# Performance work log

Hardware: AMD Instinct MI355X
Metric: run time of the kernel (lower is better)

The kernel has to match this reference:

```python
import jax, jax.numpy as jnp
import numpy as np

N_FULL = 50000
N_POOL = 12500
E_FULL = 600000
E_POOL = 150000
D = 128


def gcn_conv(x, W, b, edge_index, n):
    """GCNConv with self-loops and symmetric normalization.
    x: [n, d_in], W: [d_in, d_out], edge_index: [2, E] (src -> dst)."""
    xw = x @ W  # [n, d_out]
    loops = jnp.arange(n, dtype=edge_index.dtype)
    src = jnp.concatenate([edge_index[0], loops])
    dst = jnp.concatenate([edge_index[1], loops])
    deg = jnp.zeros((n,), dtype=xw.dtype).at[dst].add(1.0)  # >= 1 (self loops)
    dinv = jax.lax.rsqrt(deg)
    norm = (dinv[src] * dinv[dst])[:, None]  # [E+n, 1]
    out = jax.ops.segment_sum(xw[src] * norm, dst, num_segments=n)
    return out + b


def setup_inputs() -> dict:
    key = jax.random.key(0)
    ks = jax.random.split(key, 8)
    s = 1.0 / np.sqrt(D)
    return {
        "x": jnp.zeros((N_FULL, D), jnp.float32),
        "edge_index": jax.random.randint(ks[0], (2, E_FULL), 0, N_FULL, dtype=jnp.int64)
            if jax.config.jax_enable_x64 else jax.random.randint(ks[0], (2, E_FULL), 0, N_FULL).astype(jnp.int32),
        "pooled_x": jax.random.normal(ks[1], (N_POOL, D), jnp.float32),
        "pooled_edge_index": jax.random.randint(ks[2], (2, E_POOL), 0, N_POOL).astype(jnp.int32),
        "unpool_info": jnp.arange(N_POOL, dtype=jnp.int32),  # unique TopK-kept indices
        "W0": jax.random.normal(ks[3], (D, D), jnp.float32) * s,
        "b0": jnp.zeros((D,), jnp.float32),
        "W1": jax.random.normal(ks[4], (D, D), jnp.float32) * s,
        "b1": jnp.zeros((D,), jnp.float32),
        "W2": jax.random.normal(ks[5], (D, D), jnp.float32) * s,
        "b2": jnp.zeros((D,), jnp.float32),
    }


def reference(x, edge_index, pooled_x, pooled_edge_index, unpool_info,
              W0, b0, W1, b1, W2, b2):
    n = x.shape[0]
    # conv0 on the pooled graph + activation (ELU)
    h = jax.nn.elu(gcn_conv(pooled_x, W0, b0, pooled_edge_index, pooled_x.shape[0]))
    # TopKPool unpool: zero full graph, scatter pooled features to kept indices
    xf = jnp.zeros_like(x).at[unpool_info].set(h)
    # remaining convs on the full graph (dropout=0 / eval mode -> identity)
    xf = jax.nn.elu(gcn_conv(xf, W1, b1, edge_index, n))
    xf = jax.nn.elu(gcn_conv(xf, W2, b2, edge_index, n))
    return xf
```

## Files before the change

### kernel.cpp

```cpp
#include <hip/hip_runtime.h>
#include <math.h>

#define DD 128
#define CF 48
#define CP 48
#define OVF_CAP 4096

static inline int cdiv(long a, long b){ return (int)((a + b - 1) / b); }

typedef __attribute__((ext_vector_type(4))) float f32x4;
typedef __attribute__((ext_vector_type(8))) short bf16x8;
typedef __attribute__((ext_vector_type(4))) short sh4;

__device__ __forceinline__ unsigned short bf16_rn(float f){
  unsigned u = __float_as_uint(f);
  u += 0x7fffu + ((u >> 16) & 1u);
  return (unsigned short)(u >> 16);
}

__global__ void k_scatter(const int* __restrict__ src_f, const int* __restrict__ dst_f, int Ef,
                          int* __restrict__ cnt_f, int* __restrict__ ewk_f,
                          int2* __restrict__ ovf_f, int* __restrict__ novf_f,
                          const int* __restrict__ src_p, const int* __restrict__ dst_p, int Ep,
                          int* __restrict__ cnt_p, int* __restrict__ ewk_p,
                          int2* __restrict__ ovf_p, int* __restrict__ novf_p,
                          const int* __restrict__ unpool, int* __restrict__ inv, int npool){
  int e = blockIdx.x * blockDim.x + threadIdx.x;
  if (e < Ef){
    int s = src_f[e], d = dst_f[e];
    int r = atomicAdd(&cnt_f[d], 1);
    if (r < CF) ewk_f[(long)d * CF + r] = s;
    else { int o = atomicAdd(novf_f, 1); if (o < OVF_CAP) ovf_f[o] = make_int2(s, d); }
    return;
  }
  e -= Ef;
  if (e < Ep){
    int s = src_p[e], d = dst_p[e];
    int r = atomicAdd(&cnt_p[d], 1);
    if (r < CP) ewk_p[(long)d * CP + r] = s;
    else { int o = atomicAdd(novf_p, 1); if (o < OVF_CAP) ovf_p[o] = make_int2(s, d); }
    return;
  }
  e -= Ep;
  if (e < npool) inv[unpool[e]] = e;
}

template <int AMODE, bool BF16OUT>
__global__ __launch_bounds__(256, 2) void k_gemm_mfma(const void* __restrict__ Ap,
                                                      const float* __restrict__ W,
                                                      void* __restrict__ Cout, int n){
  __shared__ unsigned short Wl[2][16384];
  const int t    = threadIdx.x;
  const int lane = t & 63;
  const int wv   = t >> 6;
  const int g    = lane >> 4;
  const int r    = lane & 15;

  #pragma unroll
  for (int i = 0; i < 4; i++){
    int item = t + i * 256;
    int kq = item >> 5;
    int c4 = item & 31;
    const float* Wp = W + (long)kq * 512 + c4 * 4;
    float4 ww[4];
    #pragma unroll
    for (int kk = 0; kk < 4; kk++) ww[kk] = *(const float4*)(Wp + kk * 128);
    #pragma unroll
    for (int m = 0; m < 4; m++){
      int c = c4 * 4 + m;
      int boff = c * 256 + (((kq >> 1) ^ (c & 15)) * 16) + (kq & 1) * 8;
      sh4 hq, lq;
      #pragma unroll
      for (int kk = 0; kk < 4; kk++){
        float f = ((const float*)&ww[kk])[m];
        unsigned short hh = bf16_rn(f);
        float hf = __uint_as_float((unsigned)hh << 16);
        hq[kk] = (short)hh;
        lq[kk] = (short)bf16_rn(f - hf);
      }
      *(sh4*)((char*)(&Wl[0][0]) + boff) = hq;
      *(sh4*)((char*)(&Wl[1][0]) + boff) = lq;
    }
  }
  __syncthreads();

  const int rb = blockIdx.x * 128 + wv * 32;
  const int r0 = rb + r, r1 = rb + 16 + r;
  const bool v0 = r0 < n, v1 = r1 < n;

  f32x4 acc[2][8];
  #pragma unroll
  for (int i = 0; i < 2; i++)
    #pragma unroll
    for (int j = 0; j < 8; j++){ f32x4 z = {0.f,0.f,0.f,0.f}; acc[i][j] = z; }

  #pragma unroll
  for (int ks = 0; ks < 4; ks++){
    bf16x8 ah0, al0, ah1, al1;
    if (AMODE == 0){
      const float* pa0 = (const float*)Ap + (long)r0 * DD + g * 8;
      const float* pa1 = (const float*)Ap + (long)r1 * DD + g * 8;
      const float4 z4 = make_float4(0.f,0.f,0.f,0.f);
      float4 a00 = v0 ? *(const float4*)(pa0 + ks * 32)     : z4;
      float4 a01 = v0 ? *(const float4*)(pa0 + ks * 32 + 4) : z4;
      float4 a10 = v1 ? *(const float4*)(pa1 + ks * 32)     : z4;
      float4 a11 = v1 ? *(const float4*)(pa1 + ks * 32 + 4) : z4;
      float f0[8] = {a00.x,a00.y,a00.z,a00.w,a01.x,a01.y,a01.z,a01.w};
      float f1[8] = {a10.x,a10.y,a10.z,a10.w,a11.x,a11.y,a11.z,a11.w};
      #pragma unroll
      for (int i = 0; i < 8; i++){
        unsigned short hh = bf16_rn(f0[i]);
        ah0[i] = (short)hh;
        al0[i] = (short)bf16_rn(f0[i] - __uint_as_float((unsigned)hh << 16));
        unsigned short h1 = bf16_rn(f1[i]);
        ah1[i] = (short)h1;
        al1[i] = (short)bf16_rn(f1[i] - __uint_as_float((unsigned)h1 << 16));
      }
    } else {
      const unsigned* qa0 = (const unsigned*)Ap + (long)r0 * DD + g * 8;
      const unsigned* qa1 = (const unsigned*)Ap + (long)r1 * DD + g * 8;
      const uint4 z4 = make_uint4(0,0,0,0);
      uint4 u00 = v0 ? *(const uint4*)(qa0 + ks * 32)     : z4;
      uint4 u01 = v0 ? *(const uint4*)(qa0 + ks * 32 + 4) : z4;
      uint4 u10 = v1 ? *(const uint4*)(qa1 + ks * 32)     : z4;
      uint4 u11 = v1 ? *(const uint4*)(qa1 + ks * 32 + 4) : z4;
      unsigned uu0[8] = {u00.x,u00.y,u00.z,u00.w,u01.x,u01.y,u01.z,u01.w};
      unsigned uu1[8] = {u10.x,u10.y,u10.z,u10.w,u11.x,u11.y,u11.z,u11.w};
      #pragma unroll
      for (int i = 0; i < 8; i++){
        ah0[i] = (short)(uu0[i] & 0xffffu); al0[i] = (short)(uu0[i] >> 16);
        ah1[i] = (short)(uu1[i] & 0xffffu); al1[i] = (short)(uu1[i] >> 16);
      }
    }
    const int sb = ks * 4 + g;
    #pragma unroll
    for (int cf = 0; cf < 8; cf++){
      const int boff = (cf * 16 + r) * 256 + ((sb ^ r) * 16);
      bf16x8 wh = *(const bf16x8*)((const char*)(&Wl[0][0]) + boff);
      bf16x8 wl = *(const bf16x8*)((const char*)(&Wl[1][0]) + boff);
      acc[0][cf] = __builtin_amdgcn_mfma_f32_16x16x32_bf16(ah0, wh, acc[0][cf], 0, 0, 0);
      acc[1][cf] = __builtin_amdgcn_mfma_f32_16x16x32_bf16(ah1, wh, acc[1][cf], 0, 0, 0);
      acc[0][cf] = __builtin_amdgcn_mfma_f32_16x16x32_bf16(al0, wh, acc[0][cf], 0, 0, 0);
      acc[1][cf] = __builtin_amdgcn_mfma_f32_16x16x32_bf16(al1, wh, acc[1][cf], 0, 0, 0);
      acc[0][cf] = __builtin_amdgcn_mfma_f32_16x16x32_bf16(ah0, wl, acc[0][cf], 0, 0, 0);
      acc[1][cf] = __builtin_amdgcn_mfma_f32_16x16x32_bf16(ah1, wl, acc[1][cf], 0, 0, 0);
    }
  }

  #pragma unroll
  for (int rf = 0; rf < 2; rf++){
    #pragma unroll
    for (int cf = 0; cf < 8; cf++){
      #pragma unroll
      for (int e = 0; e < 4; e++){
        int row = rb + rf * 16 + g * 4 + e;
        if (row < n){
          float v = acc[rf][cf][e];
          if (BF16OUT)
            ((unsigned short*)Cout)[(long)row * DD + cf * 16 + r] = bf16_rn(v);
          else
            ((float*)Cout)[(long)row * DD + cf * 16 + r] = v;
        }
      }
    }
  }
}

__global__ __launch_bounds__(256) void k_agg0(const float* __restrict__ xw,
    const int* __restrict__ cnt, const int* __restrict__ ewk,
    const int2* __restrict__ ovf, const int* __restrict__ novf,
    const float* __restrict__ b, unsigned* __restrict__ outp, int n){
  int row = blockIdx.x * 4 + (threadIdx.x >> 6);
  if (row >= n) return;
  int c = (threadIdx.x & 63) * 2;
  int deg = __builtin_amdgcn_readfirstlane(cnt[row]);
  int m = deg < CP ? deg : CP;
  long base = (long)row * CP;
  float ax[4], ay[4];
  #pragma unroll
  for (int i = 0; i < 4; i++){ ax[i] = 0.f; ay[i] = 0.f; }
  int j = 0;
  for (; j + 3 < m; j += 4){
    int4 ss = *(const int4*)(ewk + base + j);
    int sa[4] = {ss.x, ss.y, ss.z, ss.w};
    #pragma unroll
    for (int i = 0; i < 4; i++){
      int s = sa[i];
      float w = rsqrtf((float)cnt[s] + 1.f);
      float2 v = *(const float2*)(xw + (long)s * DD + c);
      ax[i] += v.x * w; ay[i] += v.y * w;
    }
  }
  for (; j < m; j++){
    int s = ewk[base + j];
    float w = rsqrtf((float)cnt[s] + 1.f);
    float2 v = *(const float2*)(xw + (long)s * DD + c);
    ax[0] += v.x * w; ay[0] += v.y * w;
  }
  int no = __builtin_amdgcn_readfirstlane(novf[0]);
  if (no > 0){
    no = no < OVF_CAP ? no : OVF_CAP;
    for (int k = 0; k < no; k++){
      int2 od = ovf[k];
      if (od.y == row){
        float w = rsqrtf((float)cnt[od.x] + 1.f);
        float2 v = *(const float2*)(xw + (long)od.x * DD + c);
        ax[0] += v.x * w; ay[0] += v.y * w;
      }
    }
  }
  float sax = (ax[0]+ax[1]) + (ax[2]+ax[3]);
  float say = (ay[0]+ay[1]) + (ay[2]+ay[3]);
  float dd = rsqrtf((float)deg + 1.f);
  float2 sv = *(const float2*)(xw + (long)row * DD + c);
  float2 bb = *(const float2*)(b + c);
  float vx = sax * dd + sv.x * dd * dd + bb.x;
  float vy = say * dd + sv.y * dd * dd + bb.y;
  vx = vx > 0.f ? vx : expm1f(vx);
  vy = vy > 0.f ? vy : expm1f(vy);
  unsigned short hx = bf16_rn(vx);
  unsigned short lx = bf16_rn(vx - __uint_as_float((unsigned)hx << 16));
  unsigned short hy = bf16_rn(vy);
  unsigned short ly = bf16_rn(vy - __uint_as_float((unsigned)hy << 16));
  *(uint2*)(outp + (long)row * DD + c) =
      make_uint2((unsigned)hx | ((unsigned)lx << 16), (unsigned)hy | ((unsigned)ly << 16));
}

__global__ __launch_bounds__(256) void k_agg1(const unsigned short* __restrict__ hwb,
    const int* __restrict__ inv, const int* __restrict__ cnt,
    const int* __restrict__ ewk, const int2* __restrict__ ovf, const int* __restrict__ novf,
    const float* __restrict__ b, unsigned* __restrict__ outp, int n){
  int row = blockIdx.x * 4 + (threadIdx.x >> 6);
  if (row >= n) return;
  int c = (threadIdx.x & 63) * 2;
  int deg = __builtin_amdgcn_readfirstlane(cnt[row]);
  int m = deg < CF ? deg : CF;
  long base = (long)row * CF;
  float ax[8], ay[8];
  #pragma unroll
  for (int i = 0; i < 8; i++){ ax[i] = 0.f; ay[i] = 0.f; }
  int j = 0;
  for (; j + 7 < m; j += 8){
    int4 s0 = *(const int4*)(ewk + base + j);
    int4 s1 = *(const int4*)(ewk + base + j + 4);
    int sa[8] = {s0.x, s0.y, s0.z, s0.w, s1.x, s1.y, s1.z, s1.w};
    #pragma unroll
    for (int i = 0; i < 8; i++){
      int s = sa[i];
      int pr = inv[s];
      if (pr >= 0){
        float w = rsqrtf((float)cnt[s] + 1.f);
        unsigned v = *(const unsigned*)(hwb + (long)pr * DD + c);
        ax[i] += __uint_as_float(v << 16) * w;
        ay[i] += __uint_as_float(v & 0xffff0000u) * w;
      }
    }
  }
  for (; j < m; j++){
    int s = ewk[base + j];
    int pr = inv[s];
    if (pr >= 0){
      float w = rsqrtf((float)cnt[s] + 1.f);
      unsigned v = *(const unsigned*)(hwb + (long)pr * DD + c);
      ax[0] += __uint_as_float(v << 16) * w;
      ay[0] += __uint_as_float(v & 0xffff0000u) * w;
    }
  }
  int no = __builtin_amdgcn_readfirstlane(novf[0]);
  if (no > 0){
    no = no < OVF_CAP ? no : OVF_CAP;
    for (int k = 0; k < no; k++){
      int2 od = ovf[k];
      if (od.y == row){
        int pr = inv[od.x];
        if (pr >= 0){
          float w = rsqrtf((float)cnt[od.x] + 1.f);
          unsigned v = *(const unsigned*)(hwb + (long)pr * DD + c);
          ax[0] += __uint_as_float(v << 16) * w;
          ay[0] += __uint_as_float(v & 0xffff0000u) * w;
        }
      }
    }
  }
  float sax = ((ax[0]+ax[1])+(ax[2]+ax[3])) + ((ax[4]+ax[5])+(ax[6]+ax[7]));
  float say = ((ay[0]+ay[1])+(ay[2]+ay[3])) + ((ay[4]+ay[5])+(ay[6]+ay[7]));
  float dd = rsqrtf((float)deg + 1.f);
  int pr = inv[row];
  float sx = 0.f, sy = 0.f;
  if (pr >= 0){
    unsigned sv = *(const unsigned*)(hwb + (long)pr * DD + c);
    sx = __uint_as_float(sv << 16); sy = __uint_as_float(sv & 0xffff0000u);
  }
  float2 bb = *(const float2*)(b + c);
  float vx = sax * dd + sx * dd * dd + bb.x;
  float vy = say * dd + sy * dd * dd + bb.y;
  vx = vx > 0.f ? vx : expm1f(vx);
  vy = vy > 0.f ? vy : expm1f(vy);
  unsigned short hx = bf16_rn(vx);
  unsigned short lx = bf16_rn(vx - __uint_as_float((unsigned)hx << 16));
  unsigned short hy = bf16_rn(vy);
  unsigned short ly = bf16_rn(vy - __uint_as_float((unsigned)hy << 16));
  *(uint2*)(outp + (long)row * DD + c) =
      make_uint2((unsigned)hx | ((unsigned)lx << 16), (unsigned)hy | ((unsigned)ly << 16));
}

__global__ __launch_bounds__(256) void k_agg2(const unsigned short* __restrict__ xwb,
    const int* __restrict__ cnt, const int* __restrict__ ewk,
    const int2* __restrict__ ovf, const int* __restrict__ novf,
    const float* __restrict__ b, float* __restrict__ out, int n){
  int row = blockIdx.x * 4 + (threadIdx.x >> 6);
  if (row >= n) return;
  int c = (threadIdx.x & 63) * 2;
  int deg = __builtin_amdgcn_readfirstlane(cnt[row]);
  int m = deg < CF ? deg : CF;
  long base = (long)row * CF;
  float ax[8], ay[8];
  #pragma unroll
  for (int i = 0; i < 8; i++){ ax[i] = 0.f; ay[i] = 0.f; }
  int j = 0;
  for (; j + 7 < m; j += 8){
    int4 s0 = *(const int4*)(ewk + base + j);
    int4 s1 = *(const int4*)(ewk + base + j + 4);
    int sa[8] = {s0.x, s0.y, s0.z, s0.w, s1.x, s1.y, s1.z, s1.w};
    #pragma unroll
    for (int i = 0; i < 8; i++){
      int s = sa[i];
      float w = rsqrtf((float)cnt[s] + 1.f);
      unsigned v = *(const unsigned*)(xwb + (long)s * DD + c);
      ax[i] += __uint_as_float(v << 16) * w;
      ay[i] += __uint_as_float(v & 0xffff0000u) * w;
    }
  }
  for (; j < m; j++){
    int s = ewk[base + j];
    float w = rsqrtf((float)cnt[s] + 1.f);
    unsigned v = *(const unsigned*)(xwb + (long)s * DD + c);
    ax[0] += __uint_as_float(v << 16) * w;
    ay[0] += __uint_as_float(v & 0xffff0000u) * w;
  }
  int no = __builtin_amdgcn_readfirstlane(novf[0]);
  if (no > 0){
    no = no < OVF_CAP ? no : OVF_CAP;
    for (int k = 0; k < no; k++){
      int2 od = ovf[k];
      if (od.y == row){
        float w = rsqrtf((float)cnt[od.x] + 1.f);
        unsigned v = *(const unsigned*)(xwb + (long)od.x * DD + c);
        ax[0] += __uint_as_float(v << 16) * w;
        ay[0] += __uint_as_float(v & 0xffff0000u) * w;
      }
    }
  }
  float sax = ((ax[0]+ax[1])+(ax[2]+ax[3])) + ((ax[4]+ax[5])+(ax[6]+ax[7]));
  float say = ((ay[0]+ay[1])+(ay[2]+ay[3])) + ((ay[4]+ay[5])+(ay[6]+ay[7]));
  float dd = rsqrtf((float)deg + 1.f);
  unsigned sv = *(const unsigned*)(xwb + (long)row * DD + c);
  float sx = __uint_as_float(sv << 16), sy = __uint_as_float(sv & 0xffff0000u);
  float2 bb = *(const float2*)(b + c);
  float vx = sax * dd + sx * dd * dd + bb.x;
  float vy = say * dd + sy * dd * dd + bb.y;
  vx = vx > 0.f ? vx : expm1f(vx);
  vy = vy > 0.f ? vy : expm1f(vy);
  *(float2*)(out + (long)row * DD + c) = make_float2(vx, vy);
}

extern "C" void kernel_launch(void* const* d_in, const int* in_sizes, int n_in,
                              void* d_out, int out_size, void* d_ws, size_t ws_size,
                              hipStream_t stream) {
  const int*   edge   = (const int*)d_in[1];
  const float* px     = (const float*)d_in[2];
  const int*   pedge  = (const int*)d_in[3];
  const int*   unpool = (const int*)d_in[4];
  const float* W0 = (const float*)d_in[5]; const float* b0 = (const float*)d_in[6];
  const float* W1 = (const float*)d_in[7]; const float* b1 = (const float*)d_in[8];
  const float* W2 = (const float*)d_in[9]; const float* b2 = (const float*)d_in[10];
  const int n_full = in_sizes[0] / DD;
  const int E_full = in_sizes[1] / 2;
  const int n_pool = in_sizes[2] / DD;
  const int E_pool = in_sizes[3] / 2;
  float* out = (float*)d_out;

  char* w = (char*)d_ws;
  size_t off = 0;
  auto alloc = [&](size_t bytes) -> void* {
    void* p = (void*)(w + off);
    off += (bytes + 255) / 256 * 256;
    return p;
  };
  int* cnt_p  = (int*)alloc((size_t)n_pool * 4);
  int* cnt_f  = (int*)alloc((size_t)n_full * 4);
  int* novf2  = (int*)alloc(8);
  size_t zspan = (size_t)((char*)(novf2 + 2) - (char*)cnt_p);
  int* invm   = (int*)alloc((size_t)n_full * 4);
  int* ewk_p  = (int*)alloc((size_t)n_pool * CP * 4);
  int* ewk_f  = (int*)alloc((size_t)n_full * CF * 4);
  int2* ovf_p = (int2*)alloc((size_t)OVF_CAP * 8);
  int2* ovf_f = (int2*)alloc((size_t)OVF_CAP * 8);
  const size_t big = (size_t)n_full * DD * 4;
  float* bufA = (float*)alloc(big);
  float* bufB = (float*)alloc(big);

  const int* src_f = edge;          const int* dst_f = edge + E_full;
  const int* src_p = pedge;         const int* dst_p = pedge + E_pool;

  (void)hipMemsetAsync(cnt_p, 0, zspan, stream);
  (void)hipMemsetAsync(invm, 0xFF, (size_t)n_full * 4, stream);
  k_scatter<<<cdiv((long)E_full + E_pool + n_pool, 256), 256, 0, stream>>>(
      src_f, dst_f, E_full, cnt_f, ewk_f, ovf_f, novf2 + 1,
      src_p, dst_p, E_pool, cnt_p, ewk_p, ovf_p, novf2 + 0,
      unpool, invm, n_pool);

  float* xw0            = bufA;
  unsigned* h0p         = (unsigned*)bufB;
  unsigned short* hw1b  = (unsigned short*)bufA;
  unsigned* y1p         = (unsigned*)bufB;
  unsigned short* xw2b  = (unsigned short*)bufA;

  k_gemm_mfma<0,false><<<cdiv(n_pool,128),256,0,stream>>>(px, W0, xw0, n_pool);
  k_agg0<<<cdiv(n_pool,4),256,0,stream>>>(xw0, cnt_p, ewk_p, ovf_p, novf2 + 0, b0, h0p, n_pool);

  k_gemm_mfma<1,true><<<cdiv(n_pool,128),256,0,stream>>>(h0p, W1, hw1b, n_pool);
  k_agg1<<<cdiv(n_full,4),256,0,stream>>>(hw1b, invm, cnt_f, ewk_f, ovf_f, novf2 + 1, b1, y1p, n_full);

  k_gemm_mfma<1,true><<<cdiv(n_full,128),256,0,stream>>>(y1p, W2, xw2b, n_full);
  k_agg2<<<cdiv(n_full,4),256,0,stream>>>(xw2b, cnt_f, ewk_f, ovf_f, novf2 + 1, b2, out, n_full);
}
```

Measured before the change: 297.4 us.

## Precompute edge weights and filtered pooled-source adjacency in a two-pass build

Splits the adjacency build into a degree-count pass and a fill pass. The fill pass stores (src, rsqrt(deg+1)) pairs so the aggregation kernels no longer do a dependent cnt[] lookup and rsqrt per edge. It also builds a separate compact list for the conv1 aggregation that holds only edges whose source is a kept pooled node, already remapped to its pooled row, which removes the inv[] indirection and the wasted iterations over dropped sources. The cost is an extra kernel launch, a second pass over the edge list with more atomics, and adjacency entries twice as wide.

```diff
diff --git a/kernel.cpp b/kernel.cpp
--- a/kernel.cpp
+++ b/kernel.cpp
@@ -3,7 +3,7 @@
 
 #define DD 128
 #define CF 48
-#define CP 48
+#define C1 16
 #define OVF_CAP 4096
 
 static inline int cdiv(long a, long b){ return (int)((a + b - 1) / b); }
@@ -18,31 +18,50 @@
   return (unsigned short)(u >> 16);
 }
 
-__global__ void k_scatter(const int* __restrict__ src_f, const int* __restrict__ dst_f, int Ef,
-                          int* __restrict__ cnt_f, int* __restrict__ ewk_f,
-                          int2* __restrict__ ovf_f, int* __restrict__ novf_f,
-                          const int* __restrict__ src_p, const int* __restrict__ dst_p, int Ep,
-                          int* __restrict__ cnt_p, int* __restrict__ ewk_p,
-                          int2* __restrict__ ovf_p, int* __restrict__ novf_p,
-                          const int* __restrict__ unpool, int* __restrict__ inv, int npool){
+__global__ void k_count(const int* __restrict__ dst_f, int Ef, int* __restrict__ cnt_f,
+                        const int* __restrict__ dst_p, int Ep, int* __restrict__ cnt_p,
+                        const int* __restrict__ unpool, int* __restrict__ inv, int npool){
+  int e = blockIdx.x * blockDim.x + threadIdx.x;
+  if (e < Ef){ atomicAdd(&cnt_f[dst_f[e]], 1); return; }
+  e -= Ef;
+  if (e < Ep){ atomicAdd(&cnt_p[dst_p[e]], 1); return; }
+  e -= Ep;
+  if (e < npool) inv[unpool[e]] = e;
+}
+
+__global__ void k_fill(const int* __restrict__ src_f, const int* __restrict__ dst_f, int Ef,
+                       const int* __restrict__ cnt_f, const int* __restrict__ invm,
+                       int* __restrict__ rk2, int2* __restrict__ ew2,
+                       int4* __restrict__ ovf2, int* __restrict__ novf2,
+                       int* __restrict__ rk1, int2* __restrict__ ew1,
+                       int4* __restrict__ ovf1, int* __restrict__ novf1,
+                       const int* __restrict__ src_p, const int* __restrict__ dst_p, int Ep,
+                       const int* __restrict__ cnt_p,
+                       int* __restrict__ rk0, int2* __restrict__ ew0,
+                       int4* __restrict__ ovf0, int* __restrict__ novf0){
   int e = blockIdx.x * blockDim.x + threadIdx.x;
   if (e < Ef){
     int s = src_f[e], d = dst_f[e];
-    int r = atomicAdd(&cnt_f[d], 1);
-    if (r < CF) ewk_f[(long)d * CF + r] = s;
-    else { int o = atomicAdd(novf_f, 1); if (o < OVF_CAP) ovf_f[o] = make_int2(s, d); }
+    int w = __float_as_int(rsqrtf((float)cnt_f[s] + 1.f));
+    int r = atomicAdd(&rk2[d], 1);
+    if (r < CF) ew2[(long)d * CF + r] = make_int2(s, w);
+    else { int o = atomicAdd(novf2, 1); if (o < OVF_CAP) ovf2[o] = make_int4(s, w, d, 0); }
+    int pr = invm[s];
+    if (pr >= 0){
+      int r1 = atomicAdd(&rk1[d], 1);
+      if (r1 < C1) ew1[(long)d * C1 + r1] = make_int2(pr, w);
+      else { int o = atomicAdd(novf1, 1); if (o < OVF_CAP) ovf1[o] = make_int4(pr, w, d, 0); }
+    }
     return;
   }
   e -= Ef;
   if (e < Ep){
     int s = src_p[e], d = dst_p[e];
-    int r = atomicAdd(&cnt_p[d], 1);
-    if (r < CP) ewk_p[(long)d * CP + r] = s;
-    else { int o = atomicAdd(novf_p, 1); if (o < OVF_CAP) ovf_p[o] = make_int2(s, d); }
-    return;
-  }
-  e -= Ep;
-  if (e < npool) inv[unpool[e]] = e;
+    int w = __float_as_int(rsqrtf((float)cnt_p[s] + 1.f));
+    int r = atomicAdd(&rk0[d], 1);
+    if (r < CF) ew0[(long)d * CF + r] = make_int2(s, w);
+    else { int o = atomicAdd(novf0, 1); if (o < OVF_CAP) ovf0[o] = make_int4(s, w, d, 0); }
+  }
 }
 
 template <int AMODE, bool BF16OUT>
@@ -167,43 +186,44 @@
 }
 
 __global__ __launch_bounds__(256) void k_agg0(const float* __restrict__ xw,
-    const int* __restrict__ cnt, const int* __restrict__ ewk,
-    const int2* __restrict__ ovf, const int* __restrict__ novf,
+    const int* __restrict__ cnt, const int2* __restrict__ ew,
+    const int4* __restrict__ ovf, const int* __restrict__ novf,
     const float* __restrict__ b, unsigned* __restrict__ outp, int n){
   int row = blockIdx.x * 4 + (threadIdx.x >> 6);
   if (row >= n) return;
   int c = (threadIdx.x & 63) * 2;
   int deg = __builtin_amdgcn_readfirstlane(cnt[row]);
-  int m = deg < CP ? deg : CP;
-  long base = (long)row * CP;
+  int m = deg < CF ? deg : CF;
+  long base = (long)row * CF;
   float ax[4], ay[4];
   #pragma unroll
   for (int i = 0; i < 4; i++){ ax[i] = 0.f; ay[i] = 0.f; }
   int j = 0;
   for (; j + 3 < m; j += 4){
-    int4 ss = *(const int4*)(ewk + base + j);
-    int sa[4] = {ss.x, ss.y, ss.z, ss.w};
+    const int4* qp = (const int4*)(ew + base + j);
+    int4 q0 = qp[0], q1 = qp[1];
+    int sa[4] = {q0.x, q0.z, q1.x, q1.z};
+    int wa[4] = {q0.y, q0.w, q1.y, q1.w};
     #pragma unroll
     for (int i = 0; i < 4; i++){
-      int s = sa[i];
-      float w = rsqrtf((float)cnt[s] + 1.f);
-      float2 v = *(const float2*)(xw + (long)s * DD + c);
+      float w = __int_as_float(wa[i]);
+      float2 v = *(const float2*)(xw + (long)sa[i] * DD + c);
       ax[i] += v.x * w; ay[i] += v.y * w;
     }
   }
   for (; j < m; j++){
-    int s = ewk[base + j];
-    float w = rsqrtf((float)cnt[s] + 1.f);
-    float2 v = *(const float2*)(xw + (long)s * DD + c);
+    int2 q = ew[base + j];
+    float w = __int_as_float(q.y);
+    float2 v = *(const float2*)(xw + (long)q.x * DD + c);
     ax[0] += v.x * w; ay[0] += v.y * w;
   }
   int no = __builtin_amdgcn_readfirstlane(novf[0]);
   if (no > 0){
     no = no < OVF_CAP ? no : OVF_CAP;
     for (int k = 0; k < no; k++){
-      int2 od = ovf[k];
-      if (od.y == row){
-        float w = rsqrtf((float)cnt[od.x] + 1.f);
+      int4 od = ovf[k];
+      if (od.z == row){
+        float w = __int_as_float(od.y);
         float2 v = *(const float2*)(xw + (long)od.x * DD + c);
         ax[0] += v.x * w; ay[0] += v.y * w;
       }
@@ -227,65 +247,58 @@
 }
 
 __global__ __launch_bounds__(256) void k_agg1(const unsigned short* __restrict__ hwb,
-    const int* __restrict__ inv, const int* __restrict__ cnt,
-    const int* __restrict__ ewk, const int2* __restrict__ ovf, const int* __restrict__ novf,
+    const int* __restrict__ invm, const int* __restrict__ cnt_f,
+    const int* __restrict__ rk1, const int2* __restrict__ ew,
+    const int4* __restrict__ ovf, const int* __restrict__ novf,
     const float* __restrict__ b, unsigned* __restrict__ outp, int n){
   int row = blockIdx.x * 4 + (threadIdx.x >> 6);
   if (row >= n) return;
   int c = (threadIdx.x & 63) * 2;
-  int deg = __builtin_amdgcn_readfirstlane(cnt[row]);
-  int m = deg < CF ? deg : CF;
-  long base = (long)row * CF;
-  float ax[8], ay[8];
-  #pragma unroll
-  for (int i = 0; i < 8; i++){ ax[i] = 0.f; ay[i] = 0.f; }
+  int m1 = __builtin_amdgcn_readfirstlane(rk1[row]);
+  if (m1 > C1) m1 = C1;
+  int deg = __builtin_amdgcn_readfirstlane(cnt_f[row]);
+  long base = (long)row * C1;
+  float ax[4], ay[4];
+  #pragma unroll
+  for (int i = 0; i < 4; i++){ ax[i] = 0.f; ay[i] = 0.f; }
   int j = 0;
-  for (; j + 7 < m; j += 8){
-    int4 s0 = *(const int4*)(ewk + base + j);
-    int4 s1 = *(const int4*)(ewk + base + j + 4);
-    int sa[8] = {s0.x, s0.y, s0.z, s0.w, s1.x, s1.y, s1.z, s1.w};
-    #pragma unroll
-    for (int i = 0; i < 8; i++){
-      int s = sa[i];
-      int pr = inv[s];
-      if (pr >= 0){
-        float w = rsqrtf((float)cnt[s] + 1.f);
-        unsigned v = *(const unsigned*)(hwb + (long)pr * DD + c);
-        ax[i] += __uint_as_float(v << 16) * w;
-        ay[i] += __uint_as_float(v & 0xffff0000u) * w;
-      }
-    }
-  }
-  for (; j < m; j++){
-    int s = ewk[base + j];
-    int pr = inv[s];
-    if (pr >= 0){
-      float w = rsqrtf((float)cnt[s] + 1.f);
-      unsigned v = *(const unsigned*)(hwb + (long)pr * DD + c);
-      ax[0] += __uint_as_float(v << 16) * w;
-      ay[0] += __uint_as_float(v & 0xffff0000u) * w;
-    }
+  for (; j + 3 < m1; j += 4){
+    const int4* qp = (const int4*)(ew + base + j);
+    int4 q0 = qp[0], q1 = qp[1];
+    int sa[4] = {q0.x, q0.z, q1.x, q1.z};
+    int wa[4] = {q0.y, q0.w, q1.y, q1.w};
+    #pragma unroll
+    for (int i = 0; i < 4; i++){
+      float w = __int_as_float(wa[i]);
+      unsigned v = *(const unsigned*)(hwb + (long)sa[i] * DD + c);
+      ax[i] += __uint_as_float(v << 16) * w;
+      ay[i] += __uint_as_float(v & 0xffff0000u) * w;
+    }
+  }
+  for (; j < m1; j++){
+    int2 q = ew[base + j];
+    float w = __int_as_float(q.y);
+    unsigned v = *(const unsigned*)(hwb + (long)q.x * DD + c);
+    ax[0] += __uint_as_float(v << 16) * w;
+    ay[0] += __uint_as_float(v & 0xffff0000u) * w;
   }
   int no = __builtin_amdgcn_readfirstlane(novf[0]);
   if (no > 0){
     no = no < OVF_CAP ? no : OVF_CAP;
     for (int k = 0; k < no; k++){
-      int2 od = ovf[k];
-      if (od.y == row){
-        int pr = inv[od.x];
-        if (pr >= 0){
-          float w = rsqrtf((float)cnt[od.x] + 1.f);
-          unsigned v = *(const unsigned*)(hwb + (long)pr * DD + c);
-          ax[0] += __uint_as_float(v << 16) * w;
-          ay[0] += __uint_as_float(v & 0xffff0000u) * w;
-        }
-      }
-    }
-  }
-  float sax = ((ax[0]+ax[1])+(ax[2]+ax[3])) + ((ax[4]+ax[5])+(ax[6]+ax[7]));
-  float say = ((ay[0]+ay[1])+(ay[2]+ay[3])) + ((ay[4]+ay[5])+(ay[6]+ay[7]));
+      int4 od = ovf[k];
+      if (od.z == row){
+        float w = __int_as_float(od.y);
+        unsigned v = *(const unsigned*)(hwb + (long)od.x * DD + c);
+        ax[0] += __uint_as_float(v << 16) * w;
+        ay[0] += __uint_as_float(v & 0xffff0000u) * w;
+      }
+    }
+  }
+  float sax = (ax[0]+ax[1]) + (ax[2]+ax[3]);
+  float say = (ay[0]+ay[1]) + (ay[2]+ay[3]);
   float dd = rsqrtf((float)deg + 1.f);
-  int pr = inv[row];
+  int pr = invm[row];
   float sx = 0.f, sy = 0.f;
   if (pr >= 0){
     unsigned sv = *(const unsigned*)(hwb + (long)pr * DD + c);
@@ -305,8 +318,8 @@
 }
 
 __global__ __launch_bounds__(256) void k_agg2(const unsigned short* __restrict__ xwb,
-    const int* __restrict__ cnt, const int* __restrict__ ewk,
-    const int2* __restrict__ ovf, const int* __restrict__ novf,
+    const int* __restrict__ cnt, const int2* __restrict__ ew,
+    const int4* __restrict__ ovf, const int* __restrict__ novf,
     const float* __restrict__ b, float* __restrict__ out, int n){
   int row = blockIdx.x * 4 + (threadIdx.x >> 6);
   if (row >= n) return;
@@ -319,22 +332,22 @@
   for (int i = 0; i < 8; i++){ ax[i] = 0.f; ay[i] = 0.f; }
   int j = 0;
   for (; j + 7 < m; j += 8){
-    int4 s0 = *(const int4*)(ewk + base + j);
-    int4 s1 = *(const int4*)(ewk + base + j + 4);
-    int sa[8] = {s0.x, s0.y, s0.z, s0.w, s1.x, s1.y, s1.z, s1.w};
+    const int4* qp = (const int4*)(ew + base + j);
+    int4 q0 = qp[0], q1 = qp[1], q2 = qp[2], q3 = qp[3];
+    int sa[8] = {q0.x, q0.z, q1.x, q1.z, q2.x, q2.z, q3.x, q3.z};
+    int wa[8] = {q0.y, q0.w, q1.y, q1.w, q2.y, q2.w, q3.y, q3.w};
     #pragma unroll
     for (int i = 0; i < 8; i++){
-      int s = sa[i];
-      float w = rsqrtf((float)cnt[s] + 1.f);
-      unsigned v = *(const unsigned*)(xwb + (long)s * DD + c);
+      float w = __int_as_float(wa[i]);
+      unsigned v = *(const unsigned*)(xwb + (long)sa[i] * DD + c);
       ax[i] += __uint_as_float(v << 16) * w;
       ay[i] += __uint_as_float(v & 0xffff0000u) * w;
     }
   }
   for (; j < m; j++){
-    int s = ewk[base + j];
-    float w = rsqrtf((float)cnt[s] + 1.f);
-    unsigned v = *(const unsigned*)(xwb + (long)s * DD + c);
+    int2 q = ew[base + j];
+    float w = __int_as_float(q.y);
+    unsigned v = *(const unsigned*)(xwb + (long)q.x * DD + c);
     ax[0] += __uint_as_float(v << 16) * w;
     ay[0] += __uint_as_float(v & 0xffff0000u) * w;
   }
@@ -342,9 +355,9 @@
   if (no > 0){
     no = no < OVF_CAP ? no : OVF_CAP;
     for (int k = 0; k < no; k++){
-      int2 od = ovf[k];
-      if (od.y == row){
-        float w = rsqrtf((float)cnt[od.x] + 1.f);
+      int4 od = ovf[k];
+      if (od.z == row){
+        float w = __int_as_float(od.y);
         unsigned v = *(const unsigned*)(xwb + (long)od.x * DD + c);
         ax[0] += __uint_as_float(v << 16) * w;
         ay[0] += __uint_as_float(v & 0xffff0000u) * w;
@@ -387,15 +400,20 @@
     off += (bytes + 255) / 256 * 256;
     return p;
   };
-  int* cnt_p  = (int*)alloc((size_t)n_pool * 4);
-  int* cnt_f  = (int*)alloc((size_t)n_full * 4);
-  int* novf2  = (int*)alloc(8);
-  size_t zspan = (size_t)((char*)(novf2 + 2) - (char*)cnt_p);
-  int* invm   = (int*)alloc((size_t)n_full * 4);
-  int* ewk_p  = (int*)alloc((size_t)n_pool * CP * 4);
-  int* ewk_f  = (int*)alloc((size_t)n_full * CF * 4);
-  int2* ovf_p = (int2*)alloc((size_t)OVF_CAP * 8);
-  int2* ovf_f = (int2*)alloc((size_t)OVF_CAP * 8);
+  int* cnt_f = (int*)alloc((size_t)n_full * 4);
+  int* cnt_p = (int*)alloc((size_t)n_pool * 4);
+  int* rk2   = (int*)alloc((size_t)n_full * 4);
+  int* rk1   = (int*)alloc((size_t)n_full * 4);
+  int* rk0   = (int*)alloc((size_t)n_pool * 4);
+  int* novf3 = (int*)alloc(12);
+  size_t zspan = (size_t)((char*)(novf3 + 3) - (char*)cnt_f);
+  int* invm  = (int*)alloc((size_t)n_full * 4);
+  int2* ew2  = (int2*)alloc((size_t)n_full * CF * 8);
+  int2* ew1  = (int2*)alloc((size_t)n_full * C1 * 8);
+  int2* ew0  = (int2*)alloc((size_t)n_pool * CF * 8);
+  int4* ovf2 = (int4*)alloc((size_t)OVF_CAP * 16);
+  int4* ovf1 = (int4*)alloc((size_t)OVF_CAP * 16);
+  int4* ovf0 = (int4*)alloc((size_t)OVF_CAP * 16);
   const size_t big = (size_t)n_full * DD * 4;
   float* bufA = (float*)alloc(big);
   float* bufB = (float*)alloc(big);
@@ -403,12 +421,16 @@
   const int* src_f = edge;          const int* dst_f = edge + E_full;
   const int* src_p = pedge;         const int* dst_p = pedge + E_pool;
 
-  (void)hipMemsetAsync(cnt_p, 0, zspan, stream);
+  (void)hipMemsetAsync(cnt_f, 0, zspan, stream);
   (void)hipMemsetAsync(invm, 0xFF, (size_t)n_full * 4, stream);
-  k_scatter<<<cdiv((long)E_full + E_pool + n_pool, 256), 256, 0, stream>>>(
-      src_f, dst_f, E_full, cnt_f, ewk_f, ovf_f, novf2 + 1,
-      src_p, dst_p, E_pool, cnt_p, ewk_p, ovf_p, novf2 + 0,
-      unpool, invm, n_pool);
+  k_count<<<cdiv((long)E_full + E_pool + n_pool, 256), 256, 0, stream>>>(
+      dst_f, E_full, cnt_f, dst_p, E_pool, cnt_p, unpool, invm, n_pool);
+  k_fill<<<cdiv((long)E_full + E_pool, 256), 256, 0, stream>>>(
+      src_f, dst_f, E_full, cnt_f, invm,
+      rk2, ew2, ovf2, novf3 + 0,
+      rk1, ew1, ovf1, novf3 + 1,
+      src_p, dst_p, E_pool, cnt_p,
+      rk0, ew0, ovf0, novf3 + 2);
 
   float* xw0            = bufA;
   unsigned* h0p         = (unsigned*)bufB;
@@ -417,11 +439,11 @@
   unsigned short* xw2b  = (unsigned short*)bufA;
 
   k_gemm_mfma<0,false><<<cdiv(n_pool,128),256,0,stream>>>(px, W0, xw0, n_pool);
-  k_agg0<<<cdiv(n_pool,4),256,0,stream>>>(xw0, cnt_p, ewk_p, ovf_p, novf2 + 0, b0, h0p, n_pool);
+  k_agg0<<<cdiv(n_pool,4),256,0,stream>>>(xw0, cnt_p, ew0, ovf0, novf3 + 2, b0, h0p, n_pool);
 
   k_gemm_mfma<1,true><<<cdiv(n_pool,128),256,0,stream>>>(h0p, W1, hw1b, n_pool);
-  k_agg1<<<cdiv(n_full,4),256,0,stream>>>(hw1b, invm, cnt_f, ewk_f, ovf_f, novf2 + 1, b1, y1p, n_full);
+  k_agg1<<<cdiv(n_full,4),256,0,stream>>>(hw1b, invm, cnt_f, rk1, ew1, ovf1, novf3 + 1, b1, y1p, n_full);
 
   k_gemm_mfma<1,true><<<cdiv(n_full,128),256,0,stream>>>(y1p, W2, xw2b, n_full);
-  k_agg2<<<cdiv(n_full,4),256,0,stream>>>(xw2b, cnt_f, ewk_f, ovf_f, novf2 + 1, b2, out, n_full);
-}
+  k_agg2<<<cdiv(n_full,4),256,0,stream>>>(xw2b, cnt_f, ew2, ovf2, novf3 + 0, b2, out, n_full);
+}
```

Result: no change. 301.5 us (+1.4%).
